# Kernel tuning notes

Hardware: AMD Instinct MI355X
Metric: run time of the kernel (lower is better)

The kernel has to match this reference:

```python
import jax, jax.numpy as jnp
import numpy as np

N_NODES = 50000
N_EDGES = 800000


def gcn_conv(x, edge_index, W, b, num_nodes):
    # PyG GCNConv: out = D^-1/2 (A + I) D^-1/2 (X W) + b, with added self-loops.
    xw = x @ W  # [N, F_out]
    src, dst = edge_index[0], edge_index[1]
    loop = jnp.arange(num_nodes, dtype=src.dtype)
    src = jnp.concatenate([src, loop])
    dst = jnp.concatenate([dst, loop])
    # degree (unweighted, after self-loops) on destination nodes
    deg = jax.ops.segment_sum(jnp.ones_like(dst, dtype=xw.dtype), dst,
                              num_segments=num_nodes)
    dinv = jnp.where(deg > 0, jax.lax.rsqrt(deg), 0.0)
    norm = dinv[src] * dinv[dst]  # [E+N]
    msgs = xw[src] * norm[:, None]  # gather + scale
    out = jax.ops.segment_sum(msgs, dst, num_segments=num_nodes)  # scatter-add
    return out + b


def setup_inputs() -> dict:
    key = jax.random.key(0)
    k1, k2, k3, k4 = jax.random.split(key, 4)
    x = jax.random.normal(k1, (N_NODES, 1100), dtype=jnp.float32)
    edge_index = jax.random.randint(k2, (2, N_EDGES), 0, N_NODES, dtype=jnp.int64)
    W1 = jax.random.normal(k3, (512, 256), dtype=jnp.float32) * (1.0 / np.sqrt(512))
    b1 = jnp.zeros((256,), dtype=jnp.float32)
    W2 = jax.random.normal(k4, (256, 128), dtype=jnp.float32) * (1.0 / np.sqrt(256))
    b2 = jnp.zeros((128,), dtype=jnp.float32)
    return {"x": x, "edge_index": edge_index, "W1": W1, "b1": b1,
            "W2": W2, "b2": b2}


def reference(x, edge_index, W1, b1, W2, b2):
    protein_feature = x[:, 588:]  # [N, 512]
    h = gcn_conv(protein_feature, edge_index, W1, b1, N_NODES)
    h = jax.nn.relu(h)
    return gcn_conv(h, edge_index, W2, b2, N_NODES)
```

## Files before the change

### kernel.cpp

```cpp
#include <hip/hip_runtime.h>
#include <hip/hip_bf16.h>
#include <stdint.h>

#define N_NODES 50000
#define N_EDGES 800000
#define CAP 64

typedef __attribute__((ext_vector_type(8))) __bf16 bf16x8;
typedef __attribute__((ext_vector_type(4))) float floatx4;

__device__ __forceinline__ unsigned short f2bf(float f) {
    union { float f; unsigned u; } v; v.f = f;
    unsigned r = v.u + 0x7fffu + ((v.u >> 16) & 1u);
    return (unsigned short)(r >> 16);
}
__device__ __forceinline__ float bf2f(unsigned short h) {
    union { unsigned u; float f; } v; v.u = ((unsigned)h) << 16;
    return v.f;
}

__global__ __launch_bounds__(256) void bucket_fill_kernel(
    const int* __restrict__ src, const int* __restrict__ dst,
    unsigned* __restrict__ cnt, int* __restrict__ bucket, int nE)
{
    int i = blockIdx.x * blockDim.x + threadIdx.x;
    if (i < nE) {
        unsigned d = (unsigned)dst[i];
        unsigned s = (unsigned)src[i];
        if (d < N_NODES && s < N_NODES) {
            unsigned slot = atomicAdd(&cnt[d], 1u);
            if (slot < CAP) bucket[(size_t)d * CAP + slot] = (int)s;
        }
    }
}

__global__ __launch_bounds__(256) void dinv_kernel(
    const unsigned* __restrict__ cnt, float* __restrict__ dinv, int n)
{
    int i = blockIdx.x * blockDim.x + threadIdx.x;
    if (i < n) dinv[i] = rsqrtf((float)(cnt[i] + 1u));
}

__global__ __launch_bounds__(256) void split_w_both_kernel(
    const float* __restrict__ W1, unsigned short* __restrict__ T1h, unsigned short* __restrict__ T1l,
    const float* __restrict__ W2, unsigned short* __restrict__ T2h, unsigned short* __restrict__ T2l)
{
    const int n1 = 512 * 256;
    const int n2 = 256 * 128;
    int i = blockIdx.x * blockDim.x + threadIdx.x;
    if (i < n1) {
        int k = i >> 8;
        int n = i & 255;
        float w = W1[i];
        unsigned short hi = f2bf(w);
        unsigned short lo = f2bf(w - bf2f(hi));
        T1h[(size_t)n * 512 + k] = hi;
        T1l[(size_t)n * 512 + k] = lo;
    } else if (i < n1 + n2) {
        int j = i - n1;
        int k = j >> 7;
        int n = j & 127;
        float w = W2[j];
        unsigned short hi = f2bf(w);
        unsigned short lo = f2bf(w - bf2f(hi));
        T2h[(size_t)n * 256 + k] = hi;
        T2l[(size_t)n * 256 + k] = lo;
    }
}

#define GBM 128
#define GBK 32

__device__ __forceinline__ int chunk_off(int row, int q) {
    return row * 32 + ((q ^ ((row >> 1) & 3)) << 3);
}

template<bool AFP32, int BN>
__global__ __launch_bounds__(256, 2) void gemm_mfma_kernel(
    const float* __restrict__ Afp, int lda,
    const unsigned short* __restrict__ Ah, const unsigned short* __restrict__ Al, int apitch,
    const unsigned short* __restrict__ BTh, const unsigned short* __restrict__ BTl,
    const float* __restrict__ dinv, float* __restrict__ Y,
    int M, int K, int N)
{
    constexpr int WCOLS = BN / 2;
    constexpr int NJ    = WCOLS / 16;

    __shared__ unsigned short sAh[GBM * GBK];
    __shared__ unsigned short sAl[GBM * GBK];
    __shared__ unsigned short sBh[BN * GBK];
    __shared__ unsigned short sBl[BN * GBK];

    const int t    = threadIdx.x;
    const int bm   = blockIdx.x * GBM;
    const int bn   = blockIdx.y * BN;
    const int w    = t >> 6;
    const int lane = t & 63;
    const int wx   = w & 1;
    const int wy   = w >> 1;
    const int ml   = lane & 15;
    const int quad = lane >> 4;

    const int sr = t >> 1;
    const int q0 = (t & 1) * 2;

    floatx4 zero4 = {0.f, 0.f, 0.f, 0.f};
    floatx4 acc[4][NJ];
    #pragma unroll
    for (int i = 0; i < 4; ++i)
        #pragma unroll
        for (int j = 0; j < NJ; ++j) acc[i][j] = zero4;

    for (int k0 = 0; k0 < K; k0 += GBK) {
        if (AFP32) {
            int gr = bm + sr;
            #pragma unroll
            for (int c = 0; c < 2; ++c) {
                int q = q0 + c;
                float4 v0, v1;
                if (gr < M) {
                    const float* ap = Afp + (size_t)gr * lda + k0 + q * 8;
                    v0 = *(const float4*)(ap);
                    v1 = *(const float4*)(ap + 4);
                } else {
                    v0 = make_float4(0.f,0.f,0.f,0.f);
                    v1 = make_float4(0.f,0.f,0.f,0.f);
                }
                union { unsigned short us[8]; uint4 v; } ph, pl;
                float f[8] = {v0.x, v0.y, v0.z, v0.w, v1.x, v1.y, v1.z, v1.w};
                #pragma unroll
                for (int e = 0; e < 8; ++e) {
                    unsigned short hi = f2bf(f[e]);
                    ph.us[e] = hi;
                    pl.us[e] = f2bf(f[e] - bf2f(hi));
                }
                int off = chunk_off(sr, q);
                *(uint4*)&sAh[off] = ph.v;
                *(uint4*)&sAl[off] = pl.v;
            }
        } else {
            int gr = bm + sr;
            #pragma unroll
            for (int c = 0; c < 2; ++c) {
                int q = q0 + c;
                uint4 vh, vl;
                if (gr < M) {
                    vh = *(const uint4*)(Ah + (size_t)gr * apitch + k0 + q * 8);
                    vl = *(const uint4*)(Al + (size_t)gr * apitch + k0 + q * 8);
                } else {
                    vh = make_uint4(0,0,0,0);
                    vl = make_uint4(0,0,0,0);
                }
                int off = chunk_off(sr, q);
                *(uint4*)&sAh[off] = vh;
                *(uint4*)&sAl[off] = vl;
            }
        }
        #pragma unroll
        for (int r = 0; r < BN / 128; ++r) {
            int nr = sr + r * 128;
            const unsigned short* bh = BTh + (size_t)(bn + nr) * K + k0;
            const unsigned short* bl = BTl + (size_t)(bn + nr) * K + k0;
            #pragma unroll
            for (int c = 0; c < 2; ++c) {
                int q = q0 + c;
                uint4 vh = *(const uint4*)(bh + q * 8);
                uint4 vl = *(const uint4*)(bl + q * 8);
                int off = chunk_off(nr, q);
                *(uint4*)&sBh[off] = vh;
                *(uint4*)&sBl[off] = vl;
            }
        }
        __syncthreads();

        bf16x8 fAh[4], fAl[4];
        #pragma unroll
        for (int i = 0; i < 4; ++i) {
            int row = wy * 64 + i * 16 + ml;
            int off = chunk_off(row, quad);
            fAh[i] = *(const bf16x8*)&sAh[off];
            fAl[i] = *(const bf16x8*)&sAl[off];
        }

        #pragma unroll
        for (int j = 0; j < NJ; ++j) {
            int nrow = wx * WCOLS + j * 16 + ml;
            int off = chunk_off(nrow, quad);
            bf16x8 fBh = *(const bf16x8*)&sBh[off];
            bf16x8 fBl = *(const bf16x8*)&sBl[off];
            #pragma unroll
            for (int i = 0; i < 4; ++i) {
                floatx4 c = acc[i][j];
                c = __builtin_amdgcn_mfma_f32_16x16x32_bf16(fAh[i], fBh, c, 0, 0, 0);
                c = __builtin_amdgcn_mfma_f32_16x16x32_bf16(fAl[i], fBh, c, 0, 0, 0);
                c = __builtin_amdgcn_mfma_f32_16x16x32_bf16(fAh[i], fBl, c, 0, 0, 0);
                acc[i][j] = c;
            }
        }
        __syncthreads();
    }

    #pragma unroll
    for (int i = 0; i < 4; ++i) {
        int rb = bm + wy * 64 + i * 16 + quad * 4;
        float sc[4];
        #pragma unroll
        for (int r = 0; r < 4; ++r) sc[r] = (rb + r < M) ? dinv[rb + r] : 0.f;
        #pragma unroll
        for (int j = 0; j < NJ; ++j) {
            int col = bn + wx * WCOLS + j * 16 + ml;
            #pragma unroll
            for (int r = 0; r < 4; ++r) {
                int grow = rb + r;
                if (grow < M) Y[(size_t)grow * N + col] = acc[i][j][r] * sc[r];
            }
        }
    }
}

__global__ __launch_bounds__(256) void aggregate256_kernel(
    const float* __restrict__ Y, const int* __restrict__ bucket,
    const unsigned* __restrict__ cnt, const float* __restrict__ dinv,
    const float* __restrict__ bias,
    unsigned short* __restrict__ Hh, unsigned short* __restrict__ Hl)
{
    const int v  = blockIdx.x * 4 + (threadIdx.x >> 6);
    const int f0 = (threadIdx.x & 63) * 4;

    float4 a0 = *(const float4*)(Y + (size_t)v * 256 + f0);
    float4 a1 = make_float4(0.f,0.f,0.f,0.f);
    float4 a2 = make_float4(0.f,0.f,0.f,0.f);
    float4 a3 = make_float4(0.f,0.f,0.f,0.f);

    const int* bp = bucket + (size_t)v * CAP;
    const unsigned deg = min(cnt[v], (unsigned)CAP);
    unsigned j = 0;
    for (; j + 4 <= deg; j += 4) {
        int u0 = bp[j + 0];
        int u1 = bp[j + 1];
        int u2 = bp[j + 2];
        int u3 = bp[j + 3];
        float4 m0 = *(const float4*)(Y + (size_t)u0 * 256 + f0);
        float4 m1 = *(const float4*)(Y + (size_t)u1 * 256 + f0);
        float4 m2 = *(const float4*)(Y + (size_t)u2 * 256 + f0);
        float4 m3 = *(const float4*)(Y + (size_t)u3 * 256 + f0);
        a0.x += m0.x; a0.y += m0.y; a0.z += m0.z; a0.w += m0.w;
        a1.x += m1.x; a1.y += m1.y; a1.z += m1.z; a1.w += m1.w;
        a2.x += m2.x; a2.y += m2.y; a2.z += m2.z; a2.w += m2.w;
        a3.x += m3.x; a3.y += m3.y; a3.z += m3.z; a3.w += m3.w;
    }
    for (; j < deg; ++j) {
        float4 m = *(const float4*)(Y + (size_t)bp[j] * 256 + f0);
        a0.x += m.x; a0.y += m.y; a0.z += m.z; a0.w += m.w;
    }
    float sx = (a0.x + a1.x) + (a2.x + a3.x);
    float sy = (a0.y + a1.y) + (a2.y + a3.y);
    float sz = (a0.z + a1.z) + (a2.z + a3.z);
    float sw = (a0.w + a1.w) + (a2.w + a3.w);

    float dv = dinv[v];
    float4 b = *(const float4*)(bias + f0);
    float r[4];
    r[0] = fmaxf(sx * dv + b.x, 0.f);
    r[1] = fmaxf(sy * dv + b.y, 0.f);
    r[2] = fmaxf(sz * dv + b.z, 0.f);
    r[3] = fmaxf(sw * dv + b.w, 0.f);

    union { unsigned short us[4]; ushort4 v4; } ph, pl;
    #pragma unroll
    for (int e = 0; e < 4; ++e) {
        unsigned short hi = f2bf(r[e]);
        ph.us[e] = hi;
        pl.us[e] = f2bf(r[e] - bf2f(hi));
    }
    *(ushort4*)(Hh + (size_t)v * 256 + f0) = ph.v4;
    *(ushort4*)(Hl + (size_t)v * 256 + f0) = pl.v4;
}

__global__ __launch_bounds__(256) void aggregate128_kernel(
    const float* __restrict__ Y, const int* __restrict__ bucket,
    const unsigned* __restrict__ cnt, const float* __restrict__ dinv,
    const float* __restrict__ bias, float* __restrict__ out)
{
    const int v  = blockIdx.x * 8 + (threadIdx.x >> 5);
    const int f0 = (threadIdx.x & 31) * 4;

    float4 a0 = *(const float4*)(Y + (size_t)v * 128 + f0);
    float4 a1 = make_float4(0.f,0.f,0.f,0.f);
    float4 a2 = make_float4(0.f,0.f,0.f,0.f);
    float4 a3 = make_float4(0.f,0.f,0.f,0.f);

    const int* bp = bucket + (size_t)v * CAP;
    const unsigned deg = min(cnt[v], (unsigned)CAP);
    unsigned j = 0;
    for (; j + 4 <= deg; j += 4) {
        int u0 = bp[j + 0];
        int u1 = bp[j + 1];
        int u2 = bp[j + 2];
        int u3 = bp[j + 3];
        float4 m0 = *(const float4*)(Y + (size_t)u0 * 128 + f0);
        float4 m1 = *(const float4*)(Y + (size_t)u1 * 128 + f0);
        float4 m2 = *(const float4*)(Y + (size_t)u2 * 128 + f0);
        float4 m3 = *(const float4*)(Y + (size_t)u3 * 128 + f0);
        a0.x += m0.x; a0.y += m0.y; a0.z += m0.z; a0.w += m0.w;
        a1.x += m1.x; a1.y += m1.y; a1.z += m1.z; a1.w += m1.w;
        a2.x += m2.x; a2.y += m2.y; a2.z += m2.z; a2.w += m2.w;
        a3.x += m3.x; a3.y += m3.y; a3.z += m3.z; a3.w += m3.w;
    }
    for (; j < deg; ++j) {
        float4 m = *(const float4*)(Y + (size_t)bp[j] * 128 + f0);
        a0.x += m.x; a0.y += m.y; a0.z += m.z; a0.w += m.w;
    }
    float sx = (a0.x + a1.x) + (a2.x + a3.x);
    float sy = (a0.y + a1.y) + (a2.y + a3.y);
    float sz = (a0.z + a1.z) + (a2.z + a3.z);
    float sw = (a0.w + a1.w) + (a2.w + a3.w);

    float dv = dinv[v];
    float4 b = *(const float4*)(bias + f0);
    float4 r;
    r.x = sx * dv + b.x;
    r.y = sy * dv + b.y;
    r.z = sz * dv + b.z;
    r.w = sw * dv + b.w;
    *(float4*)(out + (size_t)v * 128 + f0) = r;
}

extern "C" void kernel_launch(void* const* d_in, const int* in_sizes, int n_in,
                              void* d_out, int out_size, void* d_ws, size_t ws_size,
                              hipStream_t stream)
{
    const float* x  = (const float*)d_in[0];
    const int*   ei = (const int*)d_in[1];
    const float* W1 = (const float*)d_in[2];
    const float* b1 = (const float*)d_in[3];
    const float* W2 = (const float*)d_in[4];
    const float* b2 = (const float*)d_in[5];
    float*       out = (float*)d_out;

    const int* e_src = ei;
    const int* e_dst = ei + N_EDGES;

    char* ws = (char*)d_ws;
    size_t o = 0;
    auto carve = [&](size_t bytes) -> char* {
        char* p = ws + o;
        o = (o + bytes + 511) & ~(size_t)511;
        return p;
    };
    unsigned*       cnt    = (unsigned*)carve((size_t)N_NODES * 4);
    float*          dinv   = (float*)carve((size_t)N_NODES * 4);
    int*            bucket = (int*)carve((size_t)N_NODES * CAP * 4);
    unsigned short* WT1h   = (unsigned short*)carve((size_t)512 * 256 * 2);
    unsigned short* WT1l   = (unsigned short*)carve((size_t)512 * 256 * 2);
    unsigned short* WT2h   = (unsigned short*)carve((size_t)256 * 128 * 2);
    unsigned short* WT2l   = (unsigned short*)carve((size_t)256 * 128 * 2);
    float*          y      = (float*)carve((size_t)N_NODES * 256 * 4);
    unsigned short* Hh     = (unsigned short*)carve((size_t)N_NODES * 256 * 2);
    unsigned short* Hl     = (unsigned short*)carve((size_t)N_NODES * 256 * 2);
    (void)ws_size;

    hipMemsetAsync(cnt, 0, (size_t)N_NODES * 4, stream);

    bucket_fill_kernel<<<(N_EDGES + 255) / 256, 256, 0, stream>>>(e_src, e_dst, cnt, bucket, N_EDGES);
    dinv_kernel<<<(N_NODES + 255) / 256, 256, 0, stream>>>(cnt, dinv, N_NODES);

    split_w_both_kernel<<<(512 * 256 + 256 * 128 + 255) / 256, 256, 0, stream>>>(
        W1, WT1h, WT1l, W2, WT2h, WT2l);

    {
        dim3 grid((N_NODES + GBM - 1) / GBM, 1);
        gemm_mfma_kernel<true, 256><<<grid, 256, 0, stream>>>(
            x + 588, 1100, nullptr, nullptr, 0, WT1h, WT1l, dinv, y,
            N_NODES, 512, 256);
    }
    aggregate256_kernel<<<N_NODES / 4, 256, 0, stream>>>(y, bucket, cnt, dinv, b1, Hh, Hl);

    {
        dim3 grid((N_NODES + GBM - 1) / GBM, 1);
        gemm_mfma_kernel<false, 128><<<grid, 256, 0, stream>>>(
            nullptr, 0, Hh, Hl, 256, WT2h, WT2l, dinv, y,
            N_NODES, 256, 128);
    }
    aggregate128_kernel<<<N_NODES / 8, 256, 0, stream>>>(y, bucket, cnt, dinv, b2, out);
}
```

Baseline: 603.6 us.

## Shrink GEMM row tile to 64 and compute dinv inline from counts

```diff
diff --git a/kernel.cpp b/kernel.cpp
--- a/kernel.cpp
+++ b/kernel.cpp
@@ -32,13 +32,6 @@
             if (slot < CAP) bucket[(size_t)d * CAP + slot] = (int)s;
         }
     }
-}
-
-__global__ __launch_bounds__(256) void dinv_kernel(
-    const unsigned* __restrict__ cnt, float* __restrict__ dinv, int n)
-{
-    int i = blockIdx.x * blockDim.x + threadIdx.x;
-    if (i < n) dinv[i] = rsqrtf((float)(cnt[i] + 1u));
 }
 
 __global__ __launch_bounds__(256) void split_w_both_kernel(
@@ -68,7 +61,7 @@
     }
 }
 
-#define GBM 128
+#define GBM 64
 #define GBK 32
 
 __device__ __forceinline__ int chunk_off(int row, int q) {
@@ -80,11 +73,12 @@
     const float* __restrict__ Afp, int lda,
     const unsigned short* __restrict__ Ah, const unsigned short* __restrict__ Al, int apitch,
     const unsigned short* __restrict__ BTh, const unsigned short* __restrict__ BTl,
-    const float* __restrict__ dinv, float* __restrict__ Y,
+    const unsigned* __restrict__ cnt, float* __restrict__ Y,
     int M, int K, int N)
 {
-    constexpr int WCOLS = BN / 2;
+    constexpr int WCOLS = BN / 4;
     constexpr int NJ    = WCOLS / 16;
+    constexpr int BCPT  = BN / 64;
 
     __shared__ unsigned short sAh[GBM * GBK];
     __shared__ unsigned short sAl[GBM * GBK];
@@ -93,16 +87,16 @@
 
     const int t    = threadIdx.x;
     const int bm   = blockIdx.x * GBM;
-    const int bn   = blockIdx.y * BN;
+    const int bn   = 0;
     const int w    = t >> 6;
     const int lane = t & 63;
-    const int wx   = w & 1;
-    const int wy   = w >> 1;
     const int ml   = lane & 15;
     const int quad = lane >> 4;
 
-    const int sr = t >> 1;
-    const int q0 = (t & 1) * 2;
+    const int asr = t >> 2;
+    const int aq  = t & 3;
+    const int bsr = (BN == 256) ? t : (t >> 1);
+    const int bq0 = (BN == 256) ? 0 : ((t & 1) * 2);
 
     floatx4 zero4 = {0.f, 0.f, 0.f, 0.f};
     floatx4 acc[4][NJ];
@@ -112,14 +106,12 @@
         for (int j = 0; j < NJ; ++j) acc[i][j] = zero4;
 
     for (int k0 = 0; k0 < K; k0 += GBK) {
-        if (AFP32) {
-            int gr = bm + sr;
-            #pragma unroll
-            for (int c = 0; c < 2; ++c) {
-                int q = q0 + c;
+        {
+            int gr = bm + asr;
+            if (AFP32) {
                 float4 v0, v1;
                 if (gr < M) {
-                    const float* ap = Afp + (size_t)gr * lda + k0 + q * 8;
+                    const float* ap = Afp + (size_t)gr * lda + k0 + aq * 8;
                     v0 = *(const float4*)(ap);
                     v1 = *(const float4*)(ap + 4);
                 } else {
@@ -134,39 +126,32 @@
                     ph.us[e] = hi;
                     pl.us[e] = f2bf(f[e] - bf2f(hi));
                 }
-                int off = chunk_off(sr, q);
+                int off = chunk_off(asr, aq);
                 *(uint4*)&sAh[off] = ph.v;
                 *(uint4*)&sAl[off] = pl.v;
-            }
-        } else {
-            int gr = bm + sr;
-            #pragma unroll
-            for (int c = 0; c < 2; ++c) {
-                int q = q0 + c;
+            } else {
                 uint4 vh, vl;
                 if (gr < M) {
-                    vh = *(const uint4*)(Ah + (size_t)gr * apitch + k0 + q * 8);
-                    vl = *(const uint4*)(Al + (size_t)gr * apitch + k0 + q * 8);
+                    vh = *(const uint4*)(Ah + (size_t)gr * apitch + k0 + aq * 8);
+                    vl = *(const uint4*)(Al + (size_t)gr * apitch + k0 + aq * 8);
                 } else {
                     vh = make_uint4(0,0,0,0);
                     vl = make_uint4(0,0,0,0);
                 }
-                int off = chunk_off(sr, q);
+                int off = chunk_off(asr, aq);
                 *(uint4*)&sAh[off] = vh;
                 *(uint4*)&sAl[off] = vl;
             }
         }
-        #pragma unroll
-        for (int r = 0; r < BN / 128; ++r) {
-            int nr = sr + r * 128;
-            const unsigned short* bh = BTh + (size_t)(bn + nr) * K + k0;
-            const unsigned short* bl = BTl + (size_t)(bn + nr) * K + k0;
+        {
+            const unsigned short* bh = BTh + (size_t)(bn + bsr) * K + k0;
+            const unsigned short* bl = BTl + (size_t)(bn + bsr) * K + k0;
             #pragma unroll
-            for (int c = 0; c < 2; ++c) {
-                int q = q0 + c;
+            for (int c = 0; c < BCPT; ++c) {
+                int q = bq0 + c;
                 uint4 vh = *(const uint4*)(bh + q * 8);
                 uint4 vl = *(const uint4*)(bl + q * 8);
-                int off = chunk_off(nr, q);
+                int off = chunk_off(bsr, q);
                 *(uint4*)&sBh[off] = vh;
                 *(uint4*)&sBl[off] = vl;
             }
@@ -176,7 +161,7 @@
         bf16x8 fAh[4], fAl[4];
         #pragma unroll
         for (int i = 0; i < 4; ++i) {
-            int row = wy * 64 + i * 16 + ml;
+            int row = i * 16 + ml;
             int off = chunk_off(row, quad);
             fAh[i] = *(const bf16x8*)&sAh[off];
             fAl[i] = *(const bf16x8*)&sAl[off];
@@ -184,7 +169,7 @@
 
         #pragma unroll
         for (int j = 0; j < NJ; ++j) {
-            int nrow = wx * WCOLS + j * 16 + ml;
+            int nrow = w * WCOLS + j * 16 + ml;
             int off = chunk_off(nrow, quad);
             bf16x8 fBh = *(const bf16x8*)&sBh[off];
             bf16x8 fBl = *(const bf16x8*)&sBl[off];
@@ -202,13 +187,14 @@
 
     #pragma unroll
     for (int i = 0; i < 4; ++i) {
-        int rb = bm + wy * 64 + i * 16 + quad * 4;
+        int rb = bm + i * 16 + quad * 4;
         float sc[4];
         #pragma unroll
-        for (int r = 0; r < 4; ++r) sc[r] = (rb + r < M) ? dinv[rb + r] : 0.f;
+        for (int r = 0; r < 4; ++r)
+            sc[r] = (rb + r < M) ? rsqrtf((float)(cnt[rb + r] + 1u)) : 0.f;
         #pragma unroll
         for (int j = 0; j < NJ; ++j) {
-            int col = bn + wx * WCOLS + j * 16 + ml;
+            int col = w * WCOLS + j * 16 + ml;
             #pragma unroll
             for (int r = 0; r < 4; ++r) {
                 int grow = rb + r;
@@ -220,8 +206,7 @@
 
 __global__ __launch_bounds__(256) void aggregate256_kernel(
     const float* __restrict__ Y, const int* __restrict__ bucket,
-    const unsigned* __restrict__ cnt, const float* __restrict__ dinv,
-    const float* __restrict__ bias,
+    const unsigned* __restrict__ cnt, const float* __restrict__ bias,
     unsigned short* __restrict__ Hh, unsigned short* __restrict__ Hl)
 {
     const int v  = blockIdx.x * 4 + (threadIdx.x >> 6);
@@ -258,7 +243,7 @@
     float sz = (a0.z + a1.z) + (a2.z + a3.z);
     float sw = (a0.w + a1.w) + (a2.w + a3.w);
 
-    float dv = dinv[v];
+    float dv = rsqrtf((float)(cnt[v] + 1u));
     float4 b = *(const float4*)(bias + f0);
     float r[4];
     r[0] = fmaxf(sx * dv + b.x, 0.f);
@@ -279,8 +264,8 @@
 
 __global__ __launch_bounds__(256) void aggregate128_kernel(
     const float* __restrict__ Y, const int* __restrict__ bucket,
-    const unsigned* __restrict__ cnt, const float* __restrict__ dinv,
-    const float* __restrict__ bias, float* __restrict__ out)
+    const unsigned* __restrict__ cnt, const float* __restrict__ bias,
+    float* __restrict__ out)
 {
     const int v  = blockIdx.x * 8 + (threadIdx.x >> 5);
     const int f0 = (threadIdx.x & 31) * 4;
@@ -316,7 +301,7 @@
     float sz = (a0.z + a1.z) + (a2.z + a3.z);
     float sw = (a0.w + a1.w) + (a2.w + a3.w);
 
-    float dv = dinv[v];
+    float dv = rsqrtf((float)(cnt[v] + 1u));
     float4 b = *(const float4*)(bias + f0);
     float4 r;
     r.x = sx * dv + b.x;
@@ -349,7 +334,6 @@
         return p;
     };
     unsigned*       cnt    = (unsigned*)carve((size_t)N_NODES * 4);
-    float*          dinv   = (float*)carve((size_t)N_NODES * 4);
     int*            bucket = (int*)carve((size_t)N_NODES * CAP * 4);
     unsigned short* WT1h   = (unsigned short*)carve((size_t)512 * 256 * 2);
     unsigned short* WT1l   = (unsigned short*)carve((size_t)512 * 256 * 2);
@@ -363,7 +347,6 @@
     hipMemsetAsync(cnt, 0, (size_t)N_NODES * 4, stream);
 
     bucket_fill_kernel<<<(N_EDGES + 255) / 256, 256, 0, stream>>>(e_src, e_dst, cnt, bucket, N_EDGES);
-    dinv_kernel<<<(N_NODES + 255) / 256, 256, 0, stream>>>(cnt, dinv, N_NODES);
 
     split_w_both_kernel<<<(512 * 256 + 256 * 128 + 255) / 256, 256, 0, stream>>>(
         W1, WT1h, WT1l, W2, WT2h, WT2l);
@@ -371,16 +354,16 @@
     {
         dim3 grid((N_NODES + GBM - 1) / GBM, 1);
         gemm_mfma_kernel<true, 256><<<grid, 256, 0, stream>>>(
-            x + 588, 1100, nullptr, nullptr, 0, WT1h, WT1l, dinv, y,
+            x + 588, 1100, nullptr, nullptr, 0, WT1h, WT1l, cnt, y,
             N_NODES, 512, 256);
     }
-    aggregate256_kernel<<<N_NODES / 4, 256, 0, stream>>>(y, bucket, cnt, dinv, b1, Hh, Hl);
+    aggregate256_kernel<<<N_NODES / 4, 256, 0, stream>>>(y, bucket, cnt, b1, Hh, Hl);
 
     {
         dim3 grid((N_NODES + GBM - 1) / GBM, 1);
         gemm_mfma_kernel<false, 128><<<grid, 256, 0, stream>>>(
-            nullptr, 0, Hh, Hl, 256, WT2h, WT2l, dinv, y,
+            nullptr, 0, Hh, Hl, 256, WT2h, WT2l, cnt, y,
             N_NODES, 256, 128);
     }
-    aggregate128_kernel<<<N_NODES / 8, 256, 0, stream>>>(y, bucket, cnt, dinv, b2, out);
-}
+    aggregate128_kernel<<<N_NODES / 8, 256, 0, stream>>>(y, bucket, cnt, b2, out);
+}
```

Result: slower. 618.4 us (+2.5%).
